# Kernel tuning notes

Hardware: AMD Instinct MI355X
Metric: run time of the kernel (lower is better)

The kernel has to match this reference:

```python
import jax, jax.numpy as jnp
import numpy as np

NUM_HEADS = 16


def setup_inputs() -> dict:
    key = jax.random.key(0)
    k1, _ = jax.random.split(key)
    B, T, C = 2, 2048, 1024
    x = jax.random.normal(k1, (B, T, C), dtype=jnp.float32)
    r_sigma = jnp.array([0.01], dtype=jnp.float32)  # learned scalar, init 0.01
    return {"x": x, "r_sigma": r_sigma}


def reference(x, r_sigma):
    B, T, C = x.shape
    H = NUM_HEADS
    hd = C // H
    xh = x.reshape(B, T, H, hd)                      # (B,T,H,hd)
    # expand_dims(x,2) - expand_dims(x,3): pairwise diff across the HEAD axis
    diff = xh[:, :, None, :, :] - xh[:, :, :, None, :]   # (B,T,H,H,hd)
    # Dist**2 == sum of squared diffs (avoid sqrt-then-square; same math)
    dist_sq = jnp.sum(diff * diff, axis=-1)          # (B,T,H,H)
    Kmat = jnp.exp(-dist_sq * r_sigma[0])            # Gaussian kernel
    # y = x + K @ x  (contract over second head axis)
    y = xh + jnp.einsum('bthg,btgd->bthd', Kmat, xh)
    return y.reshape(B, T, C)
```

## Files before the change

### kernel.cpp

```cpp
#include <hip/hip_runtime.h>


#define NH 16
#define HD 64
#define CC 1024
#define LDSROW 68

typedef float  f32x4 __attribute__((ext_vector_type(4)));
typedef _Float16 f16x4 __attribute__((ext_vector_type(4)));
typedef _Float16 f16x8 __attribute__((ext_vector_type(8)));

__global__ __launch_bounds__(256) void K_attention_MH_kernel(
    const float* __restrict__ x,
    const float* __restrict__ r_sigma,
    float* __restrict__ y,
    int ntok) {
  __shared__ __align__(16) float xs[4][NH * LDSROW];
  __shared__ __align__(16) float diag[4][NH];

  const int wid  = threadIdx.x >> 6;
  const int lane = threadIdx.x & 63;
  const int tok  = blockIdx.x * 4 + wid;
  if (tok >= ntok) return;

  const float* xp = x + (size_t)tok * CC;
  float*       yp = y + (size_t)tok * CC;
  float* xw = xs[wid];
  float* dw = diag[wid];
  const float sigma = r_sigma[0];

  const int q   = lane >> 4;
  const int col = lane & 15;

#pragma unroll
  for (int i = 0; i < 4; ++i) {
    const float4 v = reinterpret_cast<const float4*>(xp)[lane + 64 * i];
    const int p = (lane + 64 * i) * 4;
    const int h = p >> 6, d = p & 63;
    *reinterpret_cast<float4*>(&xw[h * LDSROW + d]) = v;
  }
  __builtin_amdgcn_wave_barrier();

  f32x4 g = {0.f, 0.f, 0.f, 0.f};
#pragma unroll
  for (int kc = 0; kc < 2; ++kc) {
    const float4 a0 = *reinterpret_cast<const float4*>(&xw[col * LDSROW + 8 * q + 32 * kc]);
    const float4 a1 = *reinterpret_cast<const float4*>(&xw[col * LDSROW + 8 * q + 32 * kc + 4]);
    f16x8 af;
    af[0] = (_Float16)a0.x; af[1] = (_Float16)a0.y;
    af[2] = (_Float16)a0.z; af[3] = (_Float16)a0.w;
    af[4] = (_Float16)a1.x; af[5] = (_Float16)a1.y;
    af[6] = (_Float16)a1.z; af[7] = (_Float16)a1.w;
    g = __builtin_amdgcn_mfma_f32_16x16x32_f16(af, af, g, 0, 0, 0);
  }

  if ((col >> 2) == q) {
    const int rsel = col & 3;
    const float dv = (rsel == 0) ? g[0] : (rsel == 1) ? g[1] : (rsel == 2) ? g[2] : g[3];
    dw[col] = dv;
  }
  __builtin_amdgcn_wave_barrier();
  const float dgc = dw[col];
  const f32x4 dh  = *reinterpret_cast<const f32x4*>(&dw[4 * q]);

  f16x4 ka;
  f32x4 kv;
#pragma unroll
  for (int r = 0; r < 4; ++r) {
    const float d2 = dh[r] + dgc - 2.0f * g[r];
    const float kvr = __expf(-sigma * d2);
    kv[r] = kvr;
    ka[r] = (_Float16)kvr;
  }
  (void)kv;

#pragma unroll
  for (int c = 0; c < 4; ++c) {
    float xb[4];
    f16x4 bfr;
#pragma unroll
    for (int j = 0; j < 4; ++j) {
      xb[j]  = xw[(4 * q + j) * LDSROW + 16 * c + col];
      bfr[j] = (_Float16)xb[j];
    }
    f32x4 acc = {0.f, 0.f, 0.f, 0.f};
    acc = __builtin_amdgcn_mfma_f32_16x16x16f16(ka, bfr, acc, 0, 0, 0);
#pragma unroll
    for (int r = 0; r < 4; ++r) {
      yp[(4 * q + r) * HD + 16 * c + col] = xb[r] + acc[r];
    }
  }
}

extern "C" void kernel_launch(void* const* d_in, const int* in_sizes, int n_in,
                              void* d_out, int out_size, void* d_ws, size_t ws_size,
                              hipStream_t stream) {
  const float* x = (const float*)d_in[0];
  const float* r_sigma = (const float*)d_in[1];
  float* out = (float*)d_out;
  const int ntok = in_sizes[0] / CC;
  const int blocks = (ntok + 3) / 4;
  K_attention_MH_kernel<<<blocks, 256, 0, stream>>>(x, r_sigma, out, ntok);
}
```

Baseline: 69.37 us.

## Split each token across four waves and stage output through LDS for coalesced stores

Each block now handles one token instead of four. All 256 threads cooperatively load the token, and each wave redundantly computes the 16x16 Gram matrix, then produces one 16-column slice of the output. The residual is folded into the MFMA accumulator, and results are staged in LDS so the write to global memory is one float4 per thread. This aims to cut per-wave serial work and make stores coalesced, at the cost of block-wide barriers, four times more blocks, duplicated Gram computation, and dropping the bounds check on the token count.

```diff
diff --git a/kernel.cpp b/kernel.cpp
--- a/kernel.cpp
+++ b/kernel.cpp
@@ -4,48 +4,42 @@
 #define NH 16
 #define HD 64
 #define CC 1024
-#define LDSROW 68
+#define L 68
 
-typedef float  f32x4 __attribute__((ext_vector_type(4)));
+typedef float    f32x4 __attribute__((ext_vector_type(4)));
 typedef _Float16 f16x4 __attribute__((ext_vector_type(4)));
 typedef _Float16 f16x8 __attribute__((ext_vector_type(8)));
 
 __global__ __launch_bounds__(256) void K_attention_MH_kernel(
     const float* __restrict__ x,
     const float* __restrict__ r_sigma,
-    float* __restrict__ y,
-    int ntok) {
-  __shared__ __align__(16) float xs[4][NH * LDSROW];
-  __shared__ __align__(16) float diag[4][NH];
+    float* __restrict__ y) {
+  __shared__ __align__(16) float xs[NH * L];
+  __shared__ __align__(16) float ys[NH * L];
+  __shared__ __align__(16) float dg[4][NH];
 
-  const int wid  = threadIdx.x >> 6;
-  const int lane = threadIdx.x & 63;
-  const int tok  = blockIdx.x * 4 + wid;
-  if (tok >= ntok) return;
+  const int tid  = threadIdx.x;
+  const int wid  = tid >> 6;
+  const int lane = tid & 63;
+  const int q    = lane >> 4;
+  const int col  = lane & 15;
+  const int tok  = blockIdx.x;
 
   const float* xp = x + (size_t)tok * CC;
   float*       yp = y + (size_t)tok * CC;
-  float* xw = xs[wid];
-  float* dw = diag[wid];
   const float sigma = r_sigma[0];
 
-  const int q   = lane >> 4;
-  const int col = lane & 15;
-
-#pragma unroll
-  for (int i = 0; i < 4; ++i) {
-    const float4 v = reinterpret_cast<const float4*>(xp)[lane + 64 * i];
-    const int p = (lane + 64 * i) * 4;
-    const int h = p >> 6, d = p & 63;
-    *reinterpret_cast<float4*>(&xw[h * LDSROW + d]) = v;
-  }
-  __builtin_amdgcn_wave_barrier();
+  const float4 v = reinterpret_cast<const float4*>(xp)[tid];
+  const int h  = tid >> 4;
+  const int d0 = (tid & 15) * 4;
+  *reinterpret_cast<float4*>(&xs[h * L + d0]) = v;
+  __syncthreads();
 
   f32x4 g = {0.f, 0.f, 0.f, 0.f};
 #pragma unroll
   for (int kc = 0; kc < 2; ++kc) {
-    const float4 a0 = *reinterpret_cast<const float4*>(&xw[col * LDSROW + 8 * q + 32 * kc]);
-    const float4 a1 = *reinterpret_cast<const float4*>(&xw[col * LDSROW + 8 * q + 32 * kc + 4]);
+    const float4 a0 = *reinterpret_cast<const float4*>(&xs[col * L + 8 * q + 32 * kc]);
+    const float4 a1 = *reinterpret_cast<const float4*>(&xs[col * L + 8 * q + 32 * kc + 4]);
     f16x8 af;
     af[0] = (_Float16)a0.x; af[1] = (_Float16)a0.y;
     af[2] = (_Float16)a0.z; af[3] = (_Float16)a0.w;
@@ -56,40 +50,38 @@
 
   if ((col >> 2) == q) {
     const int rsel = col & 3;
-    const float dv = (rsel == 0) ? g[0] : (rsel == 1) ? g[1] : (rsel == 2) ? g[2] : g[3];
-    dw[col] = dv;
+    dg[wid][col] = (rsel == 0) ? g[0] : (rsel == 1) ? g[1]
+                 : (rsel == 2) ? g[2] : g[3];
   }
   __builtin_amdgcn_wave_barrier();
-  const float dgc = dw[col];
-  const f32x4 dh  = *reinterpret_cast<const f32x4*>(&dw[4 * q]);
+  const float dgc = dg[wid][col];
+  const f32x4 dh  = *reinterpret_cast<const f32x4*>(&dg[wid][4 * q]);
 
   f16x4 ka;
-  f32x4 kv;
 #pragma unroll
   for (int r = 0; r < 4; ++r) {
     const float d2 = dh[r] + dgc - 2.0f * g[r];
-    const float kvr = __expf(-sigma * d2);
-    kv[r] = kvr;
-    ka[r] = (_Float16)kvr;
+    ka[r] = (_Float16)__expf(-sigma * d2);
   }
-  (void)kv;
+
+  const int dc = 16 * wid;
+  f16x4 bfr;
+  f32x4 acc;
+#pragma unroll
+  for (int j = 0; j < 4; ++j) {
+    const float xb = xs[(4 * q + j) * L + dc + col];
+    bfr[j] = (_Float16)xb;
+    acc[j] = xb;
+  }
+  acc = __builtin_amdgcn_mfma_f32_16x16x16f16(ka, bfr, acc, 0, 0, 0);
 
 #pragma unroll
-  for (int c = 0; c < 4; ++c) {
-    float xb[4];
-    f16x4 bfr;
-#pragma unroll
-    for (int j = 0; j < 4; ++j) {
-      xb[j]  = xw[(4 * q + j) * LDSROW + 16 * c + col];
-      bfr[j] = (_Float16)xb[j];
-    }
-    f32x4 acc = {0.f, 0.f, 0.f, 0.f};
-    acc = __builtin_amdgcn_mfma_f32_16x16x16f16(ka, bfr, acc, 0, 0, 0);
-#pragma unroll
-    for (int r = 0; r < 4; ++r) {
-      yp[(4 * q + r) * HD + 16 * c + col] = xb[r] + acc[r];
-    }
-  }
+  for (int r = 0; r < 4; ++r)
+    ys[(4 * q + r) * L + dc + col] = acc[r];
+  __syncthreads();
+
+  const float4 o = *reinterpret_cast<const float4*>(&ys[h * L + d0]);
+  reinterpret_cast<float4*>(yp)[tid] = o;
 }
 
 extern "C" void kernel_launch(void* const* d_in, const int* in_sizes, int n_in,
@@ -99,6 +91,5 @@
   const float* r_sigma = (const float*)d_in[1];
   float* out = (float*)d_out;
   const int ntok = in_sizes[0] / CC;
-  const int blocks = (ntok + 3) / 4;
-  K_attention_MH_kernel<<<blocks, 256, 0, stream>>>(x, r_sigma, out, ntok);
+  K_attention_MH_kernel<<<ntok, 256, 0, stream>>>(x, r_sigma, out);
 }
```

Measured after the change: 71.61 us. 1.03x slower.

## Stage MFMA output through LDS for coalesced float4 stores and fold residual into accumulator

Applied to the files above, without the earlier changes.

The output is no longer written as scattered scalar global stores. Results are written back into the per-wave LDS tile and then stored to global memory as coalesced float4 vectors. The residual x is folded in by using it as the initial MFMA accumulator, and all global loads are issued before the LDS writes. Launch bounds now request two blocks per CU, which adds a wave barrier and extra LDS traffic in exchange for wider stores.

```diff
diff --git a/kernel.cpp b/kernel.cpp
--- a/kernel.cpp
+++ b/kernel.cpp
@@ -4,19 +4,19 @@
 #define NH 16
 #define HD 64
 #define CC 1024
-#define LDSROW 68
+#define L 68
 
-typedef float  f32x4 __attribute__((ext_vector_type(4)));
+typedef float    f32x4 __attribute__((ext_vector_type(4)));
 typedef _Float16 f16x4 __attribute__((ext_vector_type(4)));
 typedef _Float16 f16x8 __attribute__((ext_vector_type(8)));
 
-__global__ __launch_bounds__(256) void K_attention_MH_kernel(
+__global__ __launch_bounds__(256, 2) void K_attention_MH_kernel(
     const float* __restrict__ x,
     const float* __restrict__ r_sigma,
     float* __restrict__ y,
     int ntok) {
-  __shared__ __align__(16) float xs[4][NH * LDSROW];
-  __shared__ __align__(16) float diag[4][NH];
+  __shared__ __align__(16) float xs[4][NH * L];
+  __shared__ __align__(16) float dg[4][NH];
 
   const int wid  = threadIdx.x >> 6;
   const int lane = threadIdx.x & 63;
@@ -26,26 +26,28 @@
   const float* xp = x + (size_t)tok * CC;
   float*       yp = y + (size_t)tok * CC;
   float* xw = xs[wid];
-  float* dw = diag[wid];
-  const float sigma = r_sigma[0];
+  float* dw = dg[wid];
 
   const int q   = lane >> 4;
   const int col = lane & 15;
 
+  float4 v[4];
 #pragma unroll
-  for (int i = 0; i < 4; ++i) {
-    const float4 v = reinterpret_cast<const float4*>(xp)[lane + 64 * i];
-    const int p = (lane + 64 * i) * 4;
-    const int h = p >> 6, d = p & 63;
-    *reinterpret_cast<float4*>(&xw[h * LDSROW + d]) = v;
-  }
+  for (int i = 0; i < 4; ++i)
+    v[i] = reinterpret_cast<const float4*>(xp)[lane + 64 * i];
+
+  const float nsig = -r_sigma[0];
+
+#pragma unroll
+  for (int i = 0; i < 4; ++i)
+    *reinterpret_cast<float4*>(&xw[(q + 4 * i) * L + 4 * col]) = v[i];
   __builtin_amdgcn_wave_barrier();
 
   f32x4 g = {0.f, 0.f, 0.f, 0.f};
 #pragma unroll
   for (int kc = 0; kc < 2; ++kc) {
-    const float4 a0 = *reinterpret_cast<const float4*>(&xw[col * LDSROW + 8 * q + 32 * kc]);
-    const float4 a1 = *reinterpret_cast<const float4*>(&xw[col * LDSROW + 8 * q + 32 * kc + 4]);
+    const float4 a0 = *reinterpret_cast<const float4*>(&xw[col * L + 8 * q + 32 * kc]);
+    const float4 a1 = *reinterpret_cast<const float4*>(&xw[col * L + 8 * q + 32 * kc + 4]);
     f16x8 af;
     af[0] = (_Float16)a0.x; af[1] = (_Float16)a0.y;
     af[2] = (_Float16)a0.z; af[3] = (_Float16)a0.w;
@@ -56,39 +58,41 @@
 
   if ((col >> 2) == q) {
     const int rsel = col & 3;
-    const float dv = (rsel == 0) ? g[0] : (rsel == 1) ? g[1] : (rsel == 2) ? g[2] : g[3];
-    dw[col] = dv;
+    dw[col] = (rsel == 0) ? g[0] : (rsel == 1) ? g[1]
+            : (rsel == 2) ? g[2] : g[3];
   }
   __builtin_amdgcn_wave_barrier();
   const float dgc = dw[col];
   const f32x4 dh  = *reinterpret_cast<const f32x4*>(&dw[4 * q]);
 
   f16x4 ka;
-  f32x4 kv;
 #pragma unroll
   for (int r = 0; r < 4; ++r) {
     const float d2 = dh[r] + dgc - 2.0f * g[r];
-    const float kvr = __expf(-sigma * d2);
-    kv[r] = kvr;
-    ka[r] = (_Float16)kvr;
+    ka[r] = (_Float16)__expf(nsig * d2);
   }
-  (void)kv;
 
 #pragma unroll
   for (int c = 0; c < 4; ++c) {
-    float xb[4];
     f16x4 bfr;
+    f32x4 acc;
 #pragma unroll
     for (int j = 0; j < 4; ++j) {
-      xb[j]  = xw[(4 * q + j) * LDSROW + 16 * c + col];
-      bfr[j] = (_Float16)xb[j];
+      const float xb = xw[(4 * q + j) * L + 16 * c + col];
+      bfr[j] = (_Float16)xb;
+      acc[j] = xb;
     }
-    f32x4 acc = {0.f, 0.f, 0.f, 0.f};
     acc = __builtin_amdgcn_mfma_f32_16x16x16f16(ka, bfr, acc, 0, 0, 0);
 #pragma unroll
-    for (int r = 0; r < 4; ++r) {
-      yp[(4 * q + r) * HD + 16 * c + col] = xb[r] + acc[r];
-    }
+    for (int r = 0; r < 4; ++r)
+      xw[(4 * q + r) * L + 16 * c + col] = acc[r];
+  }
+  __builtin_amdgcn_wave_barrier();
+
+#pragma unroll
+  for (int i = 0; i < 4; ++i) {
+    const float4 o = *reinterpret_cast<const float4*>(&xw[(q + 4 * i) * L + 4 * col]);
+    reinterpret_cast<float4*>(yp)[lane + 64 * i] = o;
   }
 }
 
```

Result: no change. 69.47 us (+0.2%).
